# Optimization experiments

Hardware: AMD Instinct MI355X
Metric: run time of the kernel (lower is better)

The kernel has to match this reference:

```python
import jax, jax.numpy as jnp
import numpy as np

B, T, C = 2, 2048, 2048
H, HKV, DH = 32, 8, 64
G = H // HKV  # kv_group_size = 4


def setup_inputs() -> dict:
    key = jax.random.key(0)
    k1, k2, k3, k4 = jax.random.split(key, 4)
    x = jax.random.normal(k1, (B, T, C), dtype=jnp.float32)
    Wq = jax.random.normal(k2, (C, C), dtype=jnp.float32) * 0.02
    Wkv = jax.random.normal(k3, (2 * HKV * DH, C), dtype=jnp.float32) * 0.02
    Wo = jax.random.normal(k4, (C, C), dtype=jnp.float32) * 0.02
    # RoPE tables: cos/sin of shape (T, DH/2)
    inv_freq = 1.0 / (10000.0 ** (jnp.arange(0, DH // 2, dtype=jnp.float32) / (DH // 2)))
    ang = jnp.arange(T, dtype=jnp.float32)[:, None] * inv_freq[None, :]  # (T, DH/2)
    return {"x": x, "cos": jnp.cos(ang), "sin": jnp.sin(ang), "Wq": Wq, "Wkv": Wkv, "Wo": Wo}


def _rotate_half(t):
    t1, t2 = jnp.split(t, 2, axis=-1)
    return jnp.concatenate([-t2, t1], axis=-1)


def reference(x, cos, sin, Wq, Wkv, Wo):
    # Projections (torch Linear: y = x @ W.T)
    q = (x @ Wq.T).reshape(B, T, H, DH).transpose(0, 2, 1, 3)      # (B,H,T,DH)
    kv = (x @ Wkv.T).reshape(B, T, 2, HKV, DH)
    k = kv[:, :, 0].transpose(0, 2, 1, 3)                          # (B,HKV,T,DH)
    v = kv[:, :, 1].transpose(0, 2, 1, 3)
    # RoPE
    cos2 = jnp.concatenate([cos, cos], axis=-1)[None, None]        # (1,1,T,DH)
    sin2 = jnp.concatenate([sin, sin], axis=-1)[None, None]
    q = q * cos2 + _rotate_half(q) * sin2
    k = k * cos2 + _rotate_half(k) * sin2
    # Grouped-query attention without materializing repeated K/V:
    # view q as (B, HKV, G, T, DH) and contract against shared K/V heads.
    qg = q.reshape(B, HKV, G, T, DH)
    scale = 1.0 / jnp.sqrt(jnp.float32(DH))
    scores = jnp.einsum("bhgqd,bhkd->bhgqk", qg, k) * scale        # (B,HKV,G,T,T)
    causal = jnp.tril(jnp.ones((T, T), dtype=bool))
    scores = jnp.where(causal[None, None, None], scores, -jnp.inf)
    attn = jax.nn.softmax(scores, axis=-1)
    out = jnp.einsum("bhgqk,bhkd->bhgqd", attn, v)                 # (B,HKV,G,T,DH)
    out = out.reshape(B, H, T, DH).transpose(0, 2, 1, 3).reshape(B, T, C)
    return out @ Wo.T
```

## Files before the change

### kernel.cpp

```cpp
#include <hip/hip_runtime.h>
#include <hip/hip_bf16.h>

#define B_    2
#define T_    2048
#define C_    2048
#define H_    32
#define HKV_  8
#define DH_   64
#define NQKV  3072
#define KOFF  2048
#define VOFF  2560

typedef __attribute__((ext_vector_type(4))) float f32x4;
typedef __attribute__((ext_vector_type(8))) short bf16x8;
typedef __attribute__((ext_vector_type(4))) short s16x4;

__device__ __forceinline__ float bf2f(short s) {
  union { unsigned u; float f; } v; v.u = ((unsigned)(unsigned short)s) << 16; return v.f;
}
__device__ __forceinline__ short f2bf(float f) {
  union { float f; unsigned u; } v; v.f = f;
  unsigned u = v.u + 0x7fffu + ((v.u >> 16) & 1u);
  return (short)(u >> 16);
}

__device__ __forceinline__ void gload_lds16(const void* g, void* l) {
  __builtin_amdgcn_global_load_lds((const __attribute__((address_space(1))) void*)g,
                                   (__attribute__((address_space(3))) void*)l, 16, 0, 0);
}

__global__ void cvt_kernel(const float* __restrict__ src, short* __restrict__ dst, int n4) {
  int i = blockIdx.x * 256 + threadIdx.x;
  if (i >= n4) return;
  const float4 v = reinterpret_cast<const float4*>(src)[i];
  s16x4 o; o[0] = f2bf(v.x); o[1] = f2bf(v.y); o[2] = f2bf(v.z); o[3] = f2bf(v.w);
  reinterpret_cast<s16x4*>(dst)[i] = o;
}

__global__ void rope_kernel(short* __restrict__ qkv, const float* __restrict__ cosT,
                            const float* __restrict__ sinT) {
  const int r = blockIdx.y;
  const int p = blockIdx.x * 256 + threadIdx.x;
  const int t = r & (T_ - 1);
  const int dd = p & 31;
  int col0; float sc;
  if (p < 1024) { int hh = p >> 5; col0 = hh * 64 + dd; sc = 0.18033688011112042f; }
  else          { int hh = (p - 1024) >> 5; col0 = KOFF + hh * 64 + dd; sc = 1.0f; }
  const float c = cosT[t * 32 + dd], s = sinT[t * 32 + dd];
  short* base = qkv + (size_t)r * NQKV;
  const float x1 = bf2f(base[col0]);
  const float x2 = bf2f(base[col0 + 32]);
  base[col0]      = f2bf((x1 * c - x2 * s) * sc);
  base[col0 + 32] = f2bf((x2 * c + x1 * s) * sc);
}

__global__ void vtrans_kernel(const short* __restrict__ qkv, short* __restrict__ vT) {
  __shared__ short tile[64][72];
  const int tid = threadIdx.x;
  const int tt = blockIdx.x, bh = blockIdx.y;
  const int b = bh >> 3, hk = bh & 7;
#pragma unroll
  for (int i = 0; i < 2; ++i) {
    int c = tid + i * 256;
    int r = c >> 3, s = c & 7;
    bf16x8 v = *reinterpret_cast<const bf16x8*>(
        qkv + ((size_t)(b * T_ + tt * 64 + r)) * NQKV + VOFF + hk * 64 + s * 8);
#pragma unroll
    for (int e = 0; e < 8; ++e) tile[s * 8 + e][r] = v[e];
  }
  __syncthreads();
#pragma unroll
  for (int i = 0; i < 2; ++i) {
    int c = tid + i * 256;
    int d = c >> 3, s = c & 7;
    bf16x8 o;
#pragma unroll
    for (int e = 0; e < 8; ++e) o[e] = tile[d][s * 8 + e];
    *reinterpret_cast<bf16x8*>(vT + ((size_t)bh * 64 + d) * T_ + tt * 64 + s * 8) = o;
  }
}

template <int OUT_BF16>
__global__ __launch_bounds__(256) void gemm_bt(const short* __restrict__ A,
                                               const short* __restrict__ Bm,
                                               void* __restrict__ Cm,
                                               int M, int N, int K) {
  __shared__ __attribute__((aligned(16))) short Alds[128 * 32];
  __shared__ __attribute__((aligned(16))) short Blds[128 * 32];
  const int tid = threadIdx.x;
  const int w = tid >> 6, lane = tid & 63, g = lane >> 4, l15 = lane & 15;
  const int wm = (w >> 1) * 64, wn = (w & 1) * 64;
  const int m0 = blockIdx.y * 128, n0 = blockIdx.x * 128;

  f32x4 acc[4][4] = {};

  for (int k0 = 0; k0 < K; k0 += 32) {
#pragma unroll
    for (int i = 0; i < 2; ++i) {
      int c = w * 128 + i * 64 + lane;
      int row = c >> 2, slot = c & 3;
      int ks = slot ^ ((row >> 1) & 3);
      gload_lds16(A + (size_t)(m0 + row) * K + k0 + ks * 8,
                  Alds + (w * 128 + i * 64) * 8);
      gload_lds16(Bm + (size_t)(n0 + row) * K + k0 + ks * 8,
                  Blds + (w * 128 + i * 64) * 8);
    }
    __syncthreads();
    bf16x8 af[4], bf[4];
#pragma unroll
    for (int mi = 0; mi < 4; ++mi) {
      int ra = wm + mi * 16 + l15;
      af[mi] = *reinterpret_cast<const bf16x8*>(Alds + ra * 32 + (g ^ ((ra >> 1) & 3)) * 8);
      int rb = wn + mi * 16 + l15;
      bf[mi] = *reinterpret_cast<const bf16x8*>(Blds + rb * 32 + (g ^ ((rb >> 1) & 3)) * 8);
    }
#pragma unroll
    for (int mi = 0; mi < 4; ++mi)
#pragma unroll
      for (int ni = 0; ni < 4; ++ni)
        acc[mi][ni] = __builtin_amdgcn_mfma_f32_16x16x32_bf16(af[mi], bf[ni], acc[mi][ni], 0, 0, 0);
    __syncthreads();
  }

#pragma unroll
  for (int mi = 0; mi < 4; ++mi)
#pragma unroll
    for (int ni = 0; ni < 4; ++ni) {
      const int m = m0 + wm + mi * 16 + g * 4;
      const int n = n0 + wn + ni * 16 + l15;
      if (OUT_BF16) {
        short* Cp = (short*)Cm;
#pragma unroll
        for (int r = 0; r < 4; ++r) Cp[(size_t)(m + r) * N + n] = f2bf(acc[mi][ni][r]);
      } else {
        float* Cp = (float*)Cm;
#pragma unroll
        for (int r = 0; r < 4; ++r) Cp[(size_t)(m + r) * N + n] = acc[mi][ni][r];
      }
    }
}

__global__ __launch_bounds__(256, 4) void attn_kernel(const short* __restrict__ qkv,
                                                      const short* __restrict__ vT,
                                                      short* __restrict__ out) {
  __shared__ __attribute__((aligned(16))) short Klds[2][64 * 64];
  __shared__ __attribute__((aligned(16))) short Vlds[2][64 * 64];
  __shared__ __attribute__((aligned(16))) short Plds[4][16 * 64];

  const int tid = threadIdx.x, w = tid >> 6, lane = tid & 63, g = lane >> 4, l15 = lane & 15;
  const int qh = blockIdx.y;
  const int b = qh >> 5, h = qh & 31, hk = h >> 2;
  const int p = blockIdx.x;
  const int qtB = 31 - p;
  const int nt = 32 - p;
  const size_t browbase = (size_t)b * T_;

  const size_t qrowA = browbase + p * 64 + w * 16 + l15;
  const size_t qrowB = browbase + qtB * 64 + w * 16 + l15;
  const bf16x8 qA0 = *reinterpret_cast<const bf16x8*>(qkv + qrowA * NQKV + h * 64 + g * 8);
  const bf16x8 qA1 = *reinterpret_cast<const bf16x8*>(qkv + qrowA * NQKV + h * 64 + 32 + g * 8);
  const bf16x8 qB0 = *reinterpret_cast<const bf16x8*>(qkv + qrowB * NQKV + h * 64 + g * 8);
  const bf16x8 qB1 = *reinterpret_cast<const bf16x8*>(qkv + qrowB * NQKV + h * 64 + 32 + g * 8);

  const short* kgbase = qkv + browbase * NQKV + KOFF + hk * 64;
  const short* vgbase = vT + ((size_t)(b * HKV_ + hk)) * 64 * T_;

  float mA = -1e30f, lA = 0.f, mB = -1e30f, lB = 0.f;
  f32x4 oA[4] = {}, oB[4] = {};

  short* const pl = &Plds[w][0];
  const int swq = (l15 & 7) << 4;
  const int qloc = w * 16 + l15;

  auto STAGE = [&](int kt, int buf) {
    const int kv0 = kt * 64;
#pragma unroll
    for (int i = 0; i < 2; ++i) {
      const int c = w * 128 + i * 64 + lane;
      const int j = c >> 3, slot = c & 7;
      gload_lds16(kgbase + (size_t)(kv0 + j) * NQKV + (slot ^ (j & 7)) * 8,
                  &Klds[buf][(w * 128 + i * 64) * 8]);
      gload_lds16(vgbase + (size_t)j * T_ + kv0 + (slot ^ (j & 7)) * 8,
                  &Vlds[buf][(w * 128 + i * 64) * 8]);
    }
  };

  auto softmax_pack = [&](f32x4* sf, float& m_run, float& l_run,
                          bf16x8& pf0, bf16x8& pf1) -> float {
    float tmax = -1e30f;
#pragma unroll
    for (int jt = 0; jt < 4; ++jt)
#pragma unroll
      for (int r = 0; r < 4; ++r) tmax = fmaxf(tmax, sf[jt][r]);
    tmax = fmaxf(tmax, __shfl_xor(tmax, 16));
    tmax = fmaxf(tmax, __shfl_xor(tmax, 32));
    const float m_new = fmaxf(m_run, tmax);
    const float corr = exp2f(m_run - m_new);
    float tsum = 0.f;
#pragma unroll
    for (int jt = 0; jt < 4; ++jt)
#pragma unroll
      for (int r = 0; r < 4; ++r) {
        float pv = exp2f(sf[jt][r] - m_new);
        sf[jt][r] = pv; tsum += pv;
      }
    tsum += __shfl_xor(tsum, 16);
    tsum += __shfl_xor(tsum, 32);
    l_run = l_run * corr + tsum;
    m_run = m_new;
#pragma unroll
    for (int jt = 0; jt < 4; ++jt) {
      s16x4 pp;
#pragma unroll
      for (int r = 0; r < 4; ++r) pp[r] = f2bf(sf[jt][r]);
      *reinterpret_cast<s16x4*>(pl + l15 * 64 + (((jt * 32 + g * 8) ^ swq) >> 1)) = pp;
    }
    pf0 = *reinterpret_cast<const bf16x8*>(pl + l15 * 64 + (((g * 16) ^ swq) >> 1));
    pf1 = *reinterpret_cast<const bf16x8*>(pl + l15 * 64 + (((64 + g * 16) ^ swq) >> 1));
    return corr;
  };

  STAGE(0, 0);
  __syncthreads();

  for (int t = 0; t < nt; ++t) {
    const int cur = t & 1;
    if (t + 1 < nt) STAGE(t + 1, cur ^ 1);
    const short* Kc = &Klds[cur][0];
    const short* Vc = &Vlds[cur][0];
    const bool doA = (t <= p);

    f32x4 s[4];
#pragma unroll
    for (int jt = 0; jt < 4; ++jt) {
      const int row = jt * 16 + l15, sw = row & 7;
      bf16x8 ka = *reinterpret_cast<const bf16x8*>(Kc + row * 64 + (g ^ sw) * 8);
      bf16x8 kb = *reinterpret_cast<const bf16x8*>(Kc + row * 64 + ((4 + g) ^ sw) * 8);
      f32x4 z = {};
      z = __builtin_amdgcn_mfma_f32_16x16x32_bf16(ka, qB0, z, 0, 0, 0);
      s[jt] = __builtin_amdgcn_mfma_f32_16x16x32_bf16(kb, qB1, z, 0, 0, 0);
    }
    if (t == nt - 1) {
#pragma unroll
      for (int jt = 0; jt < 4; ++jt)
#pragma unroll
        for (int r = 0; r < 4; ++r)
          if (jt * 16 + g * 4 + r > qloc) s[jt][r] = -1e30f;
    }
    bf16x8 pB0, pB1;
    const float corrB = softmax_pack(s, mB, lB, pB0, pB1);
#pragma unroll
    for (int dt = 0; dt < 4; ++dt) oB[dt] *= corrB;

    bf16x8 pA0, pA1;
    if (doA) {
#pragma unroll
      for (int jt = 0; jt < 4; ++jt) {
        const int row = jt * 16 + l15, sw = row & 7;
        bf16x8 ka = *reinterpret_cast<const bf16x8*>(Kc + row * 64 + (g ^ sw) * 8);
        bf16x8 kb = *reinterpret_cast<const bf16x8*>(Kc + row * 64 + ((4 + g) ^ sw) * 8);
        f32x4 z = {};
        z = __builtin_amdgcn_mfma_f32_16x16x32_bf16(ka, qA0, z, 0, 0, 0);
        s[jt] = __builtin_amdgcn_mfma_f32_16x16x32_bf16(kb, qA1, z, 0, 0, 0);
      }
      if (t == p) {
#pragma unroll
        for (int jt = 0; jt < 4; ++jt)
#pragma unroll
          for (int r = 0; r < 4; ++r)
            if (jt * 16 + g * 4 + r > qloc) s[jt][r] = -1e30f;
      }
      const float corrA = softmax_pack(s, mA, lA, pA0, pA1);
#pragma unroll
      for (int dt = 0; dt < 4; ++dt) oA[dt] *= corrA;
    }

#pragma unroll
    for (int dt = 0; dt < 4; ++dt) {
      const int row = dt * 16 + l15, sw = row & 7;
      bf16x8 v0 = *reinterpret_cast<const bf16x8*>(Vc + row * 64 + (g ^ sw) * 8);
      bf16x8 v1 = *reinterpret_cast<const bf16x8*>(Vc + row * 64 + ((4 + g) ^ sw) * 8);
      oB[dt] = __builtin_amdgcn_mfma_f32_16x16x32_bf16(v0, pB0, oB[dt], 0, 0, 0);
      oB[dt] = __builtin_amdgcn_mfma_f32_16x16x32_bf16(v1, pB1, oB[dt], 0, 0, 0);
      if (doA) {
        oA[dt] = __builtin_amdgcn_mfma_f32_16x16x32_bf16(v0, pA0, oA[dt], 0, 0, 0);
        oA[dt] = __builtin_amdgcn_mfma_f32_16x16x32_bf16(v1, pA1, oA[dt], 0, 0, 0);
      }
    }
    __syncthreads();
  }

  {
    const float inv = 1.0f / lA;
#pragma unroll
    for (int dt = 0; dt < 4; ++dt) {
      s16x4 ov;
#pragma unroll
      for (int r = 0; r < 4; ++r) ov[r] = f2bf(oA[dt][r] * inv);
      *reinterpret_cast<s16x4*>(out + qrowA * C_ + h * 64 + dt * 16 + g * 4) = ov;
    }
  }
  {
    const float inv = 1.0f / lB;
#pragma unroll
    for (int dt = 0; dt < 4; ++dt) {
      s16x4 ov;
#pragma unroll
      for (int r = 0; r < 4; ++r) ov[r] = f2bf(oB[dt][r] * inv);
      *reinterpret_cast<s16x4*>(out + qrowB * C_ + h * 64 + dt * 16 + g * 4) = ov;
    }
  }
}

extern "C" void kernel_launch(void* const* d_in, const int* in_sizes, int n_in,
                              void* d_out, int out_size, void* d_ws, size_t ws_size,
                              hipStream_t stream) {
  const float* x    = (const float*)d_in[0];
  const float* cosT = (const float*)d_in[1];
  const float* sinT = (const float*)d_in[2];
  const float* Wq   = (const float*)d_in[3];
  const float* Wkv  = (const float*)d_in[4];
  const float* Wo   = (const float*)d_in[5];

  short* xb   = (short*)d_ws;
  short* wqkv = xb + (size_t)4096 * 2048;
  short* wob  = wqkv + (size_t)3072 * 2048;
  short* qkv  = wob + (size_t)2048 * 2048;
  short* aout = qkv + (size_t)4096 * 3072;
  short* vTb  = xb;

  cvt_kernel<<<8192, 256, 0, stream>>>(x, xb, 2097152);
  cvt_kernel<<<4096, 256, 0, stream>>>(Wq, wqkv, 1048576);
  cvt_kernel<<<2048, 256, 0, stream>>>(Wkv, wqkv + (size_t)2048 * 2048, 524288);
  cvt_kernel<<<4096, 256, 0, stream>>>(Wo, wob, 1048576);

  gemm_bt<1><<<dim3(24, 32), 256, 0, stream>>>(xb, wqkv, qkv, 4096, 3072, 2048);
  rope_kernel<<<dim3(5, 4096), 256, 0, stream>>>(qkv, cosT, sinT);
  vtrans_kernel<<<dim3(32, 16), 256, 0, stream>>>(qkv, vTb);
  attn_kernel<<<dim3(16, 64), 256, 0, stream>>>(qkv, vTb, aout);
  gemm_bt<0><<<dim3(16, 32), 256, 0, stream>>>(aout, wob, (float*)d_out, 4096, 2048, 2048);
}
```

Before: 344.5 us.

## Rewrite attention with 32x32 MFMA, in-register P via permlane, lazy rescale, XCD swizzle

```diff
diff --git a/kernel.cpp b/kernel.cpp
--- a/kernel.cpp
+++ b/kernel.cpp
@@ -12,6 +12,7 @@
 #define VOFF  2560
 
 typedef __attribute__((ext_vector_type(4))) float f32x4;
+typedef __attribute__((ext_vector_type(16))) float f32x16;
 typedef __attribute__((ext_vector_type(8))) short bf16x8;
 typedef __attribute__((ext_vector_type(4))) short s16x4;
 
@@ -22,6 +23,11 @@
   union { float f; unsigned u; } v; v.f = f;
   unsigned u = v.u + 0x7fffu + ((v.u >> 16) & 1u);
   return (short)(u >> 16);
+}
+__device__ __forceinline__ unsigned pk2(float lo, float hi) {
+  union { __hip_bfloat162 b; unsigned u; } c;
+  c.b = __float22bfloat162_rn(make_float2(lo, hi));
+  return c.u;
 }
 
 __device__ __forceinline__ void gload_lds16(const void* g, void* l) {
@@ -90,7 +96,11 @@
   const int tid = threadIdx.x;
   const int w = tid >> 6, lane = tid & 63, g = lane >> 4, l15 = lane & 15;
   const int wm = (w >> 1) * 64, wn = (w & 1) * 64;
-  const int m0 = blockIdx.y * 128, n0 = blockIdx.x * 128;
+
+  int bid = blockIdx.y * gridDim.x + blockIdx.x;
+  const int nwg = gridDim.x * gridDim.y;
+  int wg = (nwg & 7) ? bid : ((bid & 7) * (nwg >> 3) + (bid >> 3));
+  const int m0 = (wg / gridDim.x) * 128, n0 = (wg % gridDim.x) * 128;
 
   f32x4 acc[4][4] = {};
 
@@ -140,37 +150,37 @@
     }
 }
 
-__global__ __launch_bounds__(256, 4) void attn_kernel(const short* __restrict__ qkv,
-                                                      const short* __restrict__ vT,
-                                                      short* __restrict__ out) {
+__global__ __launch_bounds__(256) void attn_kernel(const short* __restrict__ qkv,
+                                                   const short* __restrict__ vT,
+                                                   short* __restrict__ out) {
   __shared__ __attribute__((aligned(16))) short Klds[2][64 * 64];
   __shared__ __attribute__((aligned(16))) short Vlds[2][64 * 64];
-  __shared__ __attribute__((aligned(16))) short Plds[4][16 * 64];
-
-  const int tid = threadIdx.x, w = tid >> 6, lane = tid & 63, g = lane >> 4, l15 = lane & 15;
-  const int qh = blockIdx.y;
+
+  const int tid = threadIdx.x, w = tid >> 6, lane = tid & 63;
+  const int l31 = lane & 31, hl = lane >> 5;
+
+  const int bid = blockIdx.y * gridDim.x + blockIdx.x;
+  const int wg = (bid & 7) * 128 + (bid >> 3);
+  const int p = wg & 15, qh = wg >> 4;
   const int b = qh >> 5, h = qh & 31, hk = h >> 2;
-  const int p = blockIdx.x;
-  const int qtB = 31 - p;
+
+  const int wtile = w >> 1, wq = w & 1;
+  const int qt = wtile ? p : (31 - p);
   const int nt = 32 - p;
+  const int myend = wtile ? (p + 1) : nt;
   const size_t browbase = (size_t)b * T_;
-
-  const size_t qrowA = browbase + p * 64 + w * 16 + l15;
-  const size_t qrowB = browbase + qtB * 64 + w * 16 + l15;
-  const bf16x8 qA0 = *reinterpret_cast<const bf16x8*>(qkv + qrowA * NQKV + h * 64 + g * 8);
-  const bf16x8 qA1 = *reinterpret_cast<const bf16x8*>(qkv + qrowA * NQKV + h * 64 + 32 + g * 8);
-  const bf16x8 qB0 = *reinterpret_cast<const bf16x8*>(qkv + qrowB * NQKV + h * 64 + g * 8);
-  const bf16x8 qB1 = *reinterpret_cast<const bf16x8*>(qkv + qrowB * NQKV + h * 64 + 32 + g * 8);
-
-  const short* kgbase = qkv + browbase * NQKV + KOFF + hk * 64;
-  const short* vgbase = vT + ((size_t)(b * HKV_ + hk)) * 64 * T_;
-
-  float mA = -1e30f, lA = 0.f, mB = -1e30f, lB = 0.f;
-  f32x4 oA[4] = {}, oB[4] = {};
-
-  short* const pl = &Plds[w][0];
-  const int swq = (l15 & 7) << 4;
-  const int qloc = w * 16 + l15;
+  const size_t qrow = browbase + qt * 64 + wq * 32 + l31;
+
+  bf16x8 qf[4];
+#pragma unroll
+  for (int s = 0; s < 4; ++s)
+    qf[s] = *reinterpret_cast<const bf16x8*>(qkv + qrow * NQKV + h * 64 + s * 16 + hl * 8);
+
+  const short* kg = qkv + browbase * NQKV + KOFF + hk * 64;
+  const short* vg = vT + ((size_t)(b * HKV_ + hk)) * 64 * T_;
+
+  float m_run = -1e30f, l_run = 0.f;
+  f32x16 o0 = {}, o1 = {};
 
   auto STAGE = [&](int kt, int buf) {
     const int kv0 = kt * 64;
@@ -178,47 +188,17 @@
     for (int i = 0; i < 2; ++i) {
       const int c = w * 128 + i * 64 + lane;
       const int j = c >> 3, slot = c & 7;
-      gload_lds16(kgbase + (size_t)(kv0 + j) * NQKV + (slot ^ (j & 7)) * 8,
+      gload_lds16(kg + (size_t)(kv0 + j) * NQKV + (slot ^ (j & 7)) * 8,
                   &Klds[buf][(w * 128 + i * 64) * 8]);
-      gload_lds16(vgbase + (size_t)j * T_ + kv0 + (slot ^ (j & 7)) * 8,
+      gload_lds16(vg + (size_t)j * T_ + kv0 + (slot ^ (j & 7)) * 8,
                   &Vlds[buf][(w * 128 + i * 64) * 8]);
     }
   };
 
-  auto softmax_pack = [&](f32x4* sf, float& m_run, float& l_run,
-                          bf16x8& pf0, bf16x8& pf1) -> float {
-    float tmax = -1e30f;
-#pragma unroll
-    for (int jt = 0; jt < 4; ++jt)
-#pragma unroll
-      for (int r = 0; r < 4; ++r) tmax = fmaxf(tmax, sf[jt][r]);
-    tmax = fmaxf(tmax, __shfl_xor(tmax, 16));
-    tmax = fmaxf(tmax, __shfl_xor(tmax, 32));
-    const float m_new = fmaxf(m_run, tmax);
-    const float corr = exp2f(m_run - m_new);
-    float tsum = 0.f;
-#pragma unroll
-    for (int jt = 0; jt < 4; ++jt)
-#pragma unroll
-      for (int r = 0; r < 4; ++r) {
-        float pv = exp2f(sf[jt][r] - m_new);
-        sf[jt][r] = pv; tsum += pv;
-      }
-    tsum += __shfl_xor(tsum, 16);
-    tsum += __shfl_xor(tsum, 32);
-    l_run = l_run * corr + tsum;
-    m_run = m_new;
-#pragma unroll
-    for (int jt = 0; jt < 4; ++jt) {
-      s16x4 pp;
-#pragma unroll
-      for (int r = 0; r < 4; ++r) pp[r] = f2bf(sf[jt][r]);
-      *reinterpret_cast<s16x4*>(pl + l15 * 64 + (((jt * 32 + g * 8) ^ swq) >> 1)) = pp;
-    }
-    pf0 = *reinterpret_cast<const bf16x8*>(pl + l15 * 64 + (((g * 16) ^ swq) >> 1));
-    pf1 = *reinterpret_cast<const bf16x8*>(pl + l15 * 64 + (((64 + g * 16) ^ swq) >> 1));
-    return corr;
-  };
+#define KFRAG(TAU, S) (*reinterpret_cast<const bf16x8*>( \
+    Kc + ((TAU) * 32 + l31) * 64 + (((hl + 2 * (S)) ^ (l31 & 7)) * 8)))
+#define VFRAG(DT, S) (*reinterpret_cast<const bf16x8*>( \
+    Vc + ((DT) * 32 + l31) * 64 + (((hl + 2 * (S)) ^ (l31 & 7)) * 8)))
 
   STAGE(0, 0);
   __syncthreads();
@@ -228,88 +208,94 @@
     if (t + 1 < nt) STAGE(t + 1, cur ^ 1);
     const short* Kc = &Klds[cur][0];
     const short* Vc = &Vlds[cur][0];
-    const bool doA = (t <= p);
-
-    f32x4 s[4];
-#pragma unroll
-    for (int jt = 0; jt < 4; ++jt) {
-      const int row = jt * 16 + l15, sw = row & 7;
-      bf16x8 ka = *reinterpret_cast<const bf16x8*>(Kc + row * 64 + (g ^ sw) * 8);
-      bf16x8 kb = *reinterpret_cast<const bf16x8*>(Kc + row * 64 + ((4 + g) ^ sw) * 8);
-      f32x4 z = {};
-      z = __builtin_amdgcn_mfma_f32_16x16x32_bf16(ka, qB0, z, 0, 0, 0);
-      s[jt] = __builtin_amdgcn_mfma_f32_16x16x32_bf16(kb, qB1, z, 0, 0, 0);
-    }
-    if (t == nt - 1) {
-#pragma unroll
-      for (int jt = 0; jt < 4; ++jt)
-#pragma unroll
-        for (int r = 0; r < 4; ++r)
-          if (jt * 16 + g * 4 + r > qloc) s[jt][r] = -1e30f;
-    }
-    bf16x8 pB0, pB1;
-    const float corrB = softmax_pack(s, mB, lB, pB0, pB1);
-#pragma unroll
-    for (int dt = 0; dt < 4; ++dt) oB[dt] *= corrB;
-
-    bf16x8 pA0, pA1;
-    if (doA) {
-#pragma unroll
-      for (int jt = 0; jt < 4; ++jt) {
-        const int row = jt * 16 + l15, sw = row & 7;
-        bf16x8 ka = *reinterpret_cast<const bf16x8*>(Kc + row * 64 + (g ^ sw) * 8);
-        bf16x8 kb = *reinterpret_cast<const bf16x8*>(Kc + row * 64 + ((4 + g) ^ sw) * 8);
-        f32x4 z = {};
-        z = __builtin_amdgcn_mfma_f32_16x16x32_bf16(ka, qA0, z, 0, 0, 0);
-        s[jt] = __builtin_amdgcn_mfma_f32_16x16x32_bf16(kb, qA1, z, 0, 0, 0);
-      }
-      if (t == p) {
-#pragma unroll
-        for (int jt = 0; jt < 4; ++jt)
-#pragma unroll
-          for (int r = 0; r < 4; ++r)
-            if (jt * 16 + g * 4 + r > qloc) s[jt][r] = -1e30f;
-      }
-      const float corrA = softmax_pack(s, mA, lA, pA0, pA1);
-#pragma unroll
-      for (int dt = 0; dt < 4; ++dt) oA[dt] *= corrA;
-    }
-
-#pragma unroll
-    for (int dt = 0; dt < 4; ++dt) {
-      const int row = dt * 16 + l15, sw = row & 7;
-      bf16x8 v0 = *reinterpret_cast<const bf16x8*>(Vc + row * 64 + (g ^ sw) * 8);
-      bf16x8 v1 = *reinterpret_cast<const bf16x8*>(Vc + row * 64 + ((4 + g) ^ sw) * 8);
-      oB[dt] = __builtin_amdgcn_mfma_f32_16x16x32_bf16(v0, pB0, oB[dt], 0, 0, 0);
-      oB[dt] = __builtin_amdgcn_mfma_f32_16x16x32_bf16(v1, pB1, oB[dt], 0, 0, 0);
-      if (doA) {
-        oA[dt] = __builtin_amdgcn_mfma_f32_16x16x32_bf16(v0, pA0, oA[dt], 0, 0, 0);
-        oA[dt] = __builtin_amdgcn_mfma_f32_16x16x32_bf16(v1, pA1, oA[dt], 0, 0, 0);
-      }
+
+    if (t < myend) {
+      f32x16 st0 = {}, st1 = {};
+#pragma unroll
+      for (int s = 0; s < 4; ++s) {
+        st0 = __builtin_amdgcn_mfma_f32_32x32x16_bf16(KFRAG(0, s), qf[s], st0, 0, 0, 0);
+        st1 = __builtin_amdgcn_mfma_f32_32x32x16_bf16(KFRAG(1, s), qf[s], st1, 0, 0, 0);
+      }
+
+      if (t == myend - 1) {
+        const int qq = wq * 32 + l31;
+#pragma unroll
+        for (int r = 0; r < 16; ++r) {
+          const int j0 = (r & 3) + 8 * (r >> 2) + 4 * hl;
+          if (j0 > qq)      st0[r] = -1e30f;
+          if (j0 + 32 > qq) st1[r] = -1e30f;
+        }
+      }
+
+      float tmax = -1e30f;
+#pragma unroll
+      for (int r = 0; r < 16; ++r) tmax = fmaxf(tmax, fmaxf(st0[r], st1[r]));
+      tmax = fmaxf(tmax, __shfl_xor(tmax, 32));
+      if (__any(tmax > m_run + 8.0f)) {
+        const float m_new = fmaxf(m_run, tmax);
+        const float corr = exp2f(m_run - m_new);
+        l_run *= corr;
+#pragma unroll
+        for (int r = 0; r < 16; ++r) { o0[r] *= corr; o1[r] *= corr; }
+        m_run = m_new;
+      }
+      float tsum = 0.f;
+#pragma unroll
+      for (int r = 0; r < 16; ++r) {
+        st0[r] = exp2f(st0[r] - m_run); tsum += st0[r];
+        st1[r] = exp2f(st1[r] - m_run); tsum += st1[r];
+      }
+      tsum += __shfl_xor(tsum, 32);
+      l_run += tsum;
+
+      unsigned u0[8], u1[8];
+#pragma unroll
+      for (int k = 0; k < 8; ++k) {
+        u0[k] = pk2(st0[2 * k], st0[2 * k + 1]);
+        u1[k] = pk2(st1[2 * k], st1[2 * k + 1]);
+      }
+
+#define PV_STEP(S, UU)                                                        \
+      {                                                                       \
+        const int base_ = ((S) & 1) * 4;                                      \
+        unsigned x0 = UU[base_ + 0], y0 = UU[base_ + 2];                      \
+        unsigned x1 = UU[base_ + 1], y1 = UU[base_ + 3];                      \
+        asm volatile("v_permlane32_swap_b32 %0, %1" : "+v"(x0), "+v"(y0));    \
+        asm volatile("v_permlane32_swap_b32 %0, %1" : "+v"(x1), "+v"(y1));    \
+        union { unsigned uw[4]; bf16x8 v8; } fr_;                             \
+        fr_.uw[0] = x0; fr_.uw[1] = x1; fr_.uw[2] = y0; fr_.uw[3] = y1;       \
+        o0 = __builtin_amdgcn_mfma_f32_32x32x16_bf16(VFRAG(0, S), fr_.v8, o0, 0, 0, 0); \
+        o1 = __builtin_amdgcn_mfma_f32_32x32x16_bf16(VFRAG(1, S), fr_.v8, o1, 0, 0, 0); \
+      }
+      PV_STEP(0, u0)
+      PV_STEP(1, u0)
+      PV_STEP(2, u1)
+      PV_STEP(3, u1)
+#undef PV_STEP
     }
     __syncthreads();
   }
 
+  const float inv = 1.0f / l_run;
+  short* obase = out + qrow * C_ + h * 64;
   {
-    const float inv = 1.0f / lA;
-#pragma unroll
-    for (int dt = 0; dt < 4; ++dt) {
+#pragma unroll
+    for (int rr = 0; rr < 4; ++rr) {
       s16x4 ov;
 #pragma unroll
-      for (int r = 0; r < 4; ++r) ov[r] = f2bf(oA[dt][r] * inv);
-      *reinterpret_cast<s16x4*>(out + qrowA * C_ + h * 64 + dt * 16 + g * 4) = ov;
-    }
-  }
-  {
-    const float inv = 1.0f / lB;
-#pragma unroll
-    for (int dt = 0; dt < 4; ++dt) {
+      for (int e = 0; e < 4; ++e) ov[e] = f2bf(o0[rr * 4 + e] * inv);
+      *reinterpret_cast<s16x4*>(obase + rr * 8 + hl * 4) = ov;
+    }
+#pragma unroll
+    for (int rr = 0; rr < 4; ++rr) {
       s16x4 ov;
 #pragma unroll
-      for (int r = 0; r < 4; ++r) ov[r] = f2bf(oB[dt][r] * inv);
-      *reinterpret_cast<s16x4*>(out + qrowB * C_ + h * 64 + dt * 16 + g * 4) = ov;
-    }
-  }
+      for (int e = 0; e < 4; ++e) ov[e] = f2bf(o1[rr * 4 + e] * inv);
+      *reinterpret_cast<s16x4*>(obase + 32 + rr * 8 + hl * 4) = ov;
+    }
+  }
+#undef KFRAG
+#undef VFRAG
 }
 
 extern "C" void kernel_launch(void* const* d_in, const int* in_sizes, int n_in,
```

Result: slower. 392.4 us (+13.9%).
